# Optimization experiments

Hardware: AMD Instinct MI355X
Metric: run time of the kernel (lower is better)

Reference implementation:

```python
import jax, jax.numpy as jnp
import numpy as np

B, S, D, H = 1, 2048, 4096, 32
NEG = -1e9  # stands in for jnp.NINF in the source; finite to avoid NaNs in fully-masked rows


def _rope_tables(seq_len, dim):
    # cos/sin tables spanning the FULL hidden dim (RoPE here is applied pre-head-split)
    inv_freq = 1.0 / (10000.0 ** (np.arange(0, dim // 2, dtype=np.float32) / (dim // 2)))
    t = np.arange(seq_len, dtype=np.float32)
    freqs = np.outer(t, inv_freq)            # (S, D/2)
    emb = np.concatenate([freqs, freqs], -1)  # (S, D)
    return np.cos(emb)[None], np.sin(emb)[None]  # (1, S, D)


def setup_inputs() -> dict:
    key = jax.random.key(0)
    ks = jax.random.split(key, 5)
    cos, sin = _rope_tables(S, D)
    return {
        "hidden_state": jax.random.normal(ks[0], (B, S, D), jnp.float32),
        "attn_mask": jnp.zeros((B, 1, S, S), jnp.float32),
        "cos": jnp.asarray(cos),
        "sin": jnp.asarray(sin),
        "wq": jax.random.normal(ks[1], (D, D), jnp.float32) * 0.02,
        "wk": jax.random.normal(ks[2], (D, D), jnp.float32) * 0.02,
        "wv": jax.random.normal(ks[3], (D, D), jnp.float32) * 0.02,
        "wo": jax.random.normal(ks[4], (D, D), jnp.float32) * 0.02,
    }


def _rotate_half(x):
    x1, x2 = x[..., : x.shape[-1] // 2], x[..., x.shape[-1] // 2 :]
    return jnp.concatenate((-x2, x1), axis=-1)


def reference(hidden_state, attn_mask, cos, sin, wq, wk, wv, wo):
    b, s, d = hidden_state.shape
    h, hd = H, d // H
    # QKV projections (no bias), RoPE applied over the full hidden dim (pre-split, as in source)
    q = hidden_state @ wq
    k = hidden_state @ wk
    v = hidden_state @ wv
    q = q * cos + _rotate_half(q) * sin
    k = k * cos + _rotate_half(k) * sin
    split = lambda x: jnp.transpose(x.reshape(b, s, h, hd), (0, 2, 1, 3))  # (b,h,s,hd)
    q, k, v = split(q), split(k), split(v)
    # NOTE: source scales by sqrt(full hidden d), not sqrt(head_dim)
    scores = jnp.einsum("bhqd,bhkd->bhqk", q, k) / jnp.sqrt(jnp.float32(d))
    # source masks the LOWER triangle (incl. diagonal); replicated faithfully with finite NEG
    tri = jnp.tri(s, s, dtype=jnp.float32)
    mask = jnp.where(tri == 1, NEG, 0.0)[None, None]  # (1,1,s,s)
    scores = scores + attn_mask + mask
    attn = jax.nn.softmax(scores, axis=-1)
    out = jnp.einsum("bhqk,bhkd->bhqd", attn, v)
    out = jnp.transpose(out, (0, 2, 1, 3)).reshape(b, s, d)
    return out @ wo
```

## Files before the change

kernel.cpp:

```cpp
#include <hip/hip_runtime.h>
#include <stdint.h>


#define SS 2048
#define DD 4096
#define NH 32
#define HD 128
#define NEGV -1000000000.0f
#define LDP 136
#define LDV 72

typedef __bf16 bf16x8 __attribute__((ext_vector_type(8)));
typedef float f32x4 __attribute__((ext_vector_type(4)));

#define GLDS16(gp, lp)                                                        \
    __builtin_amdgcn_global_load_lds(                                         \
        (__attribute__((address_space(1))) uint32_t*)(uintptr_t)(gp),         \
        (__attribute__((address_space(3))) uint32_t*)(uintptr_t)(lp), 16, 0, 0)

__device__ __forceinline__ float bf2f(uint16_t u) {
    union { uint32_t i; float f; } v; v.i = ((uint32_t)u) << 16; return v.f;
}
__device__ __forceinline__ uint16_t f2bf(float f) {
    union { float f; uint32_t i; } v; v.f = f;
    uint32_t x = v.i;
    uint32_t r = (x + 0x7fffu + ((x >> 16) & 1u)) >> 16;
    return (uint16_t)r;
}

__device__ __forceinline__ void storeOut(float* C, size_t i, float v) { C[i] = v; }
__device__ __forceinline__ void storeOut(uint16_t* C, size_t i, float v) { C[i] = f2bf(v); }

__global__ void xconv_kernel(const float* __restrict__ in, uint16_t* __restrict__ out) {
    int i = blockIdx.x * blockDim.x + threadIdx.x;
    const float4* in4 = (const float4*)in;
    float4 a = in4[2 * i], b = in4[2 * i + 1];
    uint4 o;
    o.x = (uint32_t)f2bf(a.x) | ((uint32_t)f2bf(a.y) << 16);
    o.y = (uint32_t)f2bf(a.z) | ((uint32_t)f2bf(a.w) << 16);
    o.z = (uint32_t)f2bf(b.x) | ((uint32_t)f2bf(b.y) << 16);
    o.w = (uint32_t)f2bf(b.z) | ((uint32_t)f2bf(b.w) << 16);
    ((uint4*)out)[i] = o;
}

__global__ void wtrans_kernel(const float* __restrict__ in,
                              uint16_t* __restrict__ out) {
    __shared__ uint16_t tile[32][33];
    int bx = blockIdx.x * 32, by = blockIdx.y * 32;
    int tx = threadIdx.x, ty = threadIdx.y;
    #pragma unroll
    for (int i = 0; i < 32; i += 8)
        tile[ty + i][tx] = f2bf(in[(size_t)(by + ty + i) * DD + bx + tx]);
    __syncthreads();
    #pragma unroll
    for (int i = 0; i < 32; i += 8)
        out[(size_t)(bx + ty + i) * DD + by + tx] = tile[tx][ty + i];
}

template <typename OutT>
__global__ __launch_bounds__(256) void gemm_bt(const uint16_t* __restrict__ A,
                                               const uint16_t* __restrict__ Bt,
                                               OutT* __restrict__ C,
                                               int M, int N, int K) {
    __shared__ __attribute__((aligned(16))) uint16_t sA[128 * 32];
    __shared__ __attribute__((aligned(16))) uint16_t sB[128 * 32];
    int t = threadIdx.x;
    int lane = t & 63, w = t >> 6;
    int wm = (w >> 1) * 64, wn = (w & 1) * 64;
    int rowBase = blockIdx.y * 128, colBase = blockIdx.x * 128;
    f32x4 acc[4][4] = {};

    int lr = lane & 15;
    int kq = (lane >> 4) * 8;

    for (int k0 = 0; k0 < K; k0 += 32) {
        __syncthreads();
        #pragma unroll
        for (int p = 0; p < 2; ++p) {
            int c = p * 256 + t;
            int r = c >> 2;
            int cc = (c & 3) * 8;
            GLDS16(&A[(size_t)(rowBase + r) * K + k0 + cc], &sA[c * 8]);
            GLDS16(&Bt[(size_t)(colBase + r) * K + k0 + cc], &sB[c * 8]);
        }
        __syncthreads();

        bf16x8 af[4], bfr[4];
        #pragma unroll
        for (int i = 0; i < 4; ++i) {
            af[i]  = *(const bf16x8*)(&sA[(wm + i * 16 + lr) * 32 + kq]);
            bfr[i] = *(const bf16x8*)(&sB[(wn + i * 16 + lr) * 32 + kq]);
        }
        #pragma unroll
        for (int mt = 0; mt < 4; ++mt)
            #pragma unroll
            for (int nt = 0; nt < 4; ++nt)
                acc[mt][nt] = __builtin_amdgcn_mfma_f32_16x16x32_bf16(
                    af[mt], bfr[nt], acc[mt][nt], 0, 0, 0);
    }

    int q = lane >> 4;
    #pragma unroll
    for (int mt = 0; mt < 4; ++mt)
        #pragma unroll
        for (int nt = 0; nt < 4; ++nt)
            #pragma unroll
            for (int r = 0; r < 4; ++r) {
                int row = rowBase + wm + mt * 16 + q * 4 + r;
                int col = colBase + wn + nt * 16 + lr;
                storeOut(C, (size_t)row * N + col, acc[mt][nt][r]);
            }
}

__global__ void rope_kernel(uint16_t* __restrict__ q, uint16_t* __restrict__ k,
                            const float* __restrict__ cosb,
                            const float* __restrict__ sinb) {
    int idx = blockIdx.x * blockDim.x + threadIdx.x;
    int s = idx >> 11;
    int d = idx & 2047;
    size_t i0 = (size_t)s * DD + d, i1 = i0 + 2048;
    float c0 = cosb[i0], c1 = cosb[i1];
    float s0 = sinb[i0], s1 = sinb[i1];
    float q0 = bf2f(q[i0]), q1 = bf2f(q[i1]);
    q[i0] = f2bf(q0 * c0 - q1 * s0);
    q[i1] = f2bf(q1 * c1 + q0 * s1);
    float k0 = bf2f(k[i0]), k1 = bf2f(k[i1]);
    k[i0] = f2bf(k0 * c0 - k1 * s0);
    k[i1] = f2bf(k1 * c1 + k0 * s1);
}

__global__ __launch_bounds__(256) void fattn_kernel(
    const uint16_t* __restrict__ Q, const uint16_t* __restrict__ K,
    const uint16_t* __restrict__ VT, const float* __restrict__ mask,
    uint16_t* __restrict__ O)
{
    __shared__ __attribute__((aligned(16))) uint16_t sQ[64 * LDP];
    __shared__ __attribute__((aligned(16))) uint16_t sK[64 * LDP];
    __shared__ __attribute__((aligned(16))) uint16_t sVt[HD * LDV];
    __shared__ __attribute__((aligned(16))) uint16_t sP[64 * LDV];
    __shared__ float sAlpha[64];
    __shared__ float sL[64];

    int h = blockIdx.y, q0 = blockIdx.x * 64;
    int base = h * HD;
    int t = threadIdx.x;
    int lane = t & 63, w = t >> 6;
    int lr = lane & 15, quad = lane >> 4;
    int mw = w * 16;

    for (int c = t; c < 64 * 16; c += 256) {
        int m = c >> 4, dc = (c & 15) * 8;
        *(uint4*)(&sQ[m * LDP + dc]) =
            *(const uint4*)(&Q[(size_t)(q0 + m) * DD + base + dc]);
    }

    f32x4 oacc[2][4] = {};
    float m_pr[4], l_run[4];
    #pragma unroll
    for (int r = 0; r < 4; ++r) { m_pr[r] = -3.0e38f; l_run[r] = 0.f; }

    int kt_lo = (q0 == SS - 64) ? 0 : blockIdx.x;
    for (int kt = kt_lo; kt < SS / 64; ++kt) {
        __syncthreads();
        for (int c = t; c < 64 * 16; c += 256) {
            int r = c >> 4, dc = (c & 15) * 8;
            *(uint4*)(&sK[r * LDP + dc]) =
                *(const uint4*)(&K[(size_t)(kt * 64 + r) * DD + base + dc]);
        }
        for (int c = t; c < 128 * 8; c += 256) {
            int r = c >> 3, dc = (c & 7) * 8;
            *(uint4*)(&sVt[r * LDV + dc]) =
                *(const uint4*)(&VT[(size_t)(base + r) * SS + kt * 64 + dc]);
        }
        __syncthreads();

        f32x4 sacc[4] = {};
        __builtin_amdgcn_s_setprio(1);
        #pragma unroll
        for (int kc = 0; kc < 4; ++kc) {
            bf16x8 af = *(const bf16x8*)(&sQ[(mw + lr) * LDP + kc * 32 + quad * 8]);
            #pragma unroll
            for (int nt = 0; nt < 4; ++nt) {
                bf16x8 bfr = *(const bf16x8*)(&sK[(nt * 16 + lr) * LDP + kc * 32 + quad * 8]);
                sacc[nt] = __builtin_amdgcn_mfma_f32_16x16x32_bf16(af, bfr, sacc[nt], 0, 0, 0);
            }
        }
        __builtin_amdgcn_s_setprio(0);

        float sc[4][4];
        #pragma unroll
        for (int nt = 0; nt < 4; ++nt) {
            int kk = kt * 64 + nt * 16 + lr;
            #pragma unroll
            for (int r = 0; r < 4; ++r) {
                int qrow = q0 + mw + quad * 4 + r;
                float s = sacc[nt][r] * 0.015625f + mask[(size_t)qrow * SS + kk];
                if (kk <= qrow) s += NEGV;
                sc[nt][r] = s;
            }
        }

        float mnew[4], alpha[4];
        #pragma unroll
        for (int r = 0; r < 4; ++r) {
            float mx = sc[0][r];
            #pragma unroll
            for (int nt = 1; nt < 4; ++nt) mx = fmaxf(mx, sc[nt][r]);
            #pragma unroll
            for (int off = 1; off < 16; off <<= 1)
                mx = fmaxf(mx, __shfl_xor(mx, off));
            mnew[r] = fmaxf(m_pr[r], mx);
            alpha[r] = __expf(m_pr[r] - mnew[r]);
            m_pr[r] = mnew[r];
        }

        float ps[4] = {0.f, 0.f, 0.f, 0.f};
        #pragma unroll
        for (int nt = 0; nt < 4; ++nt) {
            #pragma unroll
            for (int r = 0; r < 4; ++r) {
                float p = __expf(sc[nt][r] - mnew[r]);
                ps[r] += p;
                sP[(mw + quad * 4 + r) * LDV + nt * 16 + lr] = f2bf(p);
            }
        }
        #pragma unroll
        for (int r = 0; r < 4; ++r) {
            #pragma unroll
            for (int off = 1; off < 16; off <<= 1)
                ps[r] += __shfl_xor(ps[r], off);
            l_run[r] = l_run[r] * alpha[r] + ps[r];
            if (lr == 0) sAlpha[mw + quad * 4 + r] = alpha[r];
        }
        __syncthreads();

        float a_col[4];
        #pragma unroll
        for (int nt = 0; nt < 4; ++nt) a_col[nt] = sAlpha[nt * 16 + lr];
        #pragma unroll
        for (int dt = 0; dt < 2; ++dt)
            #pragma unroll
            for (int nt = 0; nt < 4; ++nt)
                #pragma unroll
                for (int r = 0; r < 4; ++r)
                    oacc[dt][nt][r] *= a_col[nt];
        __builtin_amdgcn_s_setprio(1);
        #pragma unroll
        for (int kc = 0; kc < 2; ++kc) {
            bf16x8 bfr[4];
            #pragma unroll
            for (int nt = 0; nt < 4; ++nt)
                bfr[nt] = *(const bf16x8*)(&sP[(nt * 16 + lr) * LDV + kc * 32 + quad * 8]);
            #pragma unroll
            for (int dt = 0; dt < 2; ++dt) {
                bf16x8 af = *(const bf16x8*)(&sVt[((2 * w + dt) * 16 + lr) * LDV + kc * 32 + quad * 8]);
                #pragma unroll
                for (int nt = 0; nt < 4; ++nt)
                    oacc[dt][nt] = __builtin_amdgcn_mfma_f32_16x16x32_bf16(af, bfr[nt], oacc[dt][nt], 0, 0, 0);
            }
        }
        __builtin_amdgcn_s_setprio(0);
    }

    #pragma unroll
    for (int r = 0; r < 4; ++r)
        if (lr == 0) sL[mw + quad * 4 + r] = l_run[r];
    __syncthreads();

    float linv[4];
    #pragma unroll
    for (int nt = 0; nt < 4; ++nt) linv[nt] = 1.f / sL[nt * 16 + lr];
    #pragma unroll
    for (int dt = 0; dt < 2; ++dt) {
        int ddl = (2 * w + dt) * 16 + quad * 4;
        #pragma unroll
        for (int nt = 0; nt < 4; ++nt) {
            int ml = nt * 16 + lr;
            #pragma unroll
            for (int r = 0; r < 4; ++r)
                sK[ml * LDP + ddl + r] = f2bf(oacc[dt][nt][r] * linv[nt]);
        }
    }
    __syncthreads();
    for (int c = t; c < 64 * 16; c += 256) {
        int m = c >> 4, dc = (c & 15) * 8;
        *(uint4*)(&O[(size_t)(q0 + m) * DD + base + dc]) =
            *(const uint4*)(&sK[m * LDP + dc]);
    }
}

extern "C" void kernel_launch(void* const* d_in, const int* in_sizes, int n_in,
                              void* d_out, int out_size, void* d_ws, size_t ws_size,
                              hipStream_t stream) {
    const float* X    = (const float*)d_in[0];
    const float* mask = (const float*)d_in[1];
    const float* cosb = (const float*)d_in[2];
    const float* sinb = (const float*)d_in[3];
    const float* wq   = (const float*)d_in[4];
    const float* wk   = (const float*)d_in[5];
    const float* wv   = (const float*)d_in[6];
    const float* wo   = (const float*)d_in[7];
    float* out = (float*)d_out;

    char* ws = (char*)d_ws;
    uint16_t* Wt  = (uint16_t*)ws;
    uint16_t* Xbf = (uint16_t*)(ws + (size_t)33554432);
    uint16_t* Q   = Xbf + (size_t)SS * DD;
    uint16_t* Kb  = Q  + (size_t)SS * DD;
    uint16_t* VT  = Kb + (size_t)SS * DD;
    uint16_t* AO  = Xbf;

    dim3 tgrid(DD / 32, DD / 32), tblock(32, 8);
    dim3 ggrid(DD / 128, SS / 128), gblock(256);

    xconv_kernel<<<(SS * DD) / (256 * 8), 256, 0, stream>>>(X, Xbf);

    wtrans_kernel<<<tgrid, tblock, 0, stream>>>(wq, Wt);
    gemm_bt<<<ggrid, gblock, 0, stream>>>(Xbf, Wt, Q, SS, DD, DD);
    wtrans_kernel<<<tgrid, tblock, 0, stream>>>(wk, Wt);
    gemm_bt<<<ggrid, gblock, 0, stream>>>(Xbf, Wt, Kb, SS, DD, DD);
    wtrans_kernel<<<tgrid, tblock, 0, stream>>>(wv, Wt);
    gemm_bt<<<dim3(SS / 128, DD / 128), gblock, 0, stream>>>(Wt, Xbf, VT, DD, SS, DD);

    rope_kernel<<<(SS * 2048) / 256, 256, 0, stream>>>(Q, Kb, cosb, sinb);

    fattn_kernel<<<dim3(SS / 64, NH), 256, 0, stream>>>(Q, Kb, VT, mask, AO);

    wtrans_kernel<<<tgrid, tblock, 0, stream>>>(wo, Wt);
    gemm_bt<<<ggrid, gblock, 0, stream>>>(AO, Wt, out, SS, DD, DD);
}
```

Before: 1.111 ms.

## Pair causal query blocks per workgroup and stage mask tiles in LDS

Attention blocks now each handle two query tiles chosen as complementary pairs (j and 29-j, plus 30/31 together), so every workgroup does a similar amount of key-tile work under the triangular mask. The grid shrinks to 512 one-dimensional workgroups with a block-index swizzle spread across XCDs. The additive mask tile is also loaded into LDS with coalesced float4 loads instead of strided per-element global reads. This costs extra LDS (about 17 KB) and half as many workgroups in flight, which may lower occupancy.

```diff
diff --git a/kernel.cpp b/kernel.cpp
--- a/kernel.cpp
+++ b/kernel.cpp
@@ -9,6 +9,7 @@
 #define NEGV -1000000000.0f
 #define LDP 136
 #define LDV 72
+#define LDM 68
 
 typedef __bf16 bf16x8 __attribute__((ext_vector_type(8)));
 typedef float f32x4 __attribute__((ext_vector_type(4)));
@@ -138,154 +139,167 @@
     __shared__ __attribute__((aligned(16))) uint16_t sK[64 * LDP];
     __shared__ __attribute__((aligned(16))) uint16_t sVt[HD * LDV];
     __shared__ __attribute__((aligned(16))) uint16_t sP[64 * LDV];
+    __shared__ __attribute__((aligned(16))) float sM[64 * LDM];
     __shared__ float sAlpha[64];
     __shared__ float sL[64];
 
-    int h = blockIdx.y, q0 = blockIdx.x * 64;
+    int p = blockIdx.x;
+    int virt = (p & 7) * 64 + (p >> 3);
+    int h = virt >> 4, j = virt & 15;
     int base = h * HD;
     int t = threadIdx.x;
     int lane = t & 63, w = t >> 6;
     int lr = lane & 15, quad = lane >> 4;
     int mw = w * 16;
 
-    for (int c = t; c < 64 * 16; c += 256) {
-        int m = c >> 4, dc = (c & 15) * 8;
-        *(uint4*)(&sQ[m * LDP + dc]) =
-            *(const uint4*)(&Q[(size_t)(q0 + m) * DD + base + dc]);
-    }
-
-    f32x4 oacc[2][4] = {};
-    float m_pr[4], l_run[4];
-    #pragma unroll
-    for (int r = 0; r < 4; ++r) { m_pr[r] = -3.0e38f; l_run[r] = 0.f; }
-
-    int kt_lo = (q0 == SS - 64) ? 0 : blockIdx.x;
-    for (int kt = kt_lo; kt < SS / 64; ++kt) {
+    for (int item = 0; item < 2; ++item) {
+        int qb = (j < 15) ? (item ? 29 - j : j) : (30 + item);
+        int q0 = qb * 64;
+
+        for (int c = t; c < 64 * 16; c += 256) {
+            int m = c >> 4, dc = (c & 15) * 8;
+            *(uint4*)(&sQ[m * LDP + dc]) =
+                *(const uint4*)(&Q[(size_t)(q0 + m) * DD + base + dc]);
+        }
+
+        f32x4 oacc[2][4] = {};
+        float m_pr[4], l_run[4];
+        #pragma unroll
+        for (int r = 0; r < 4; ++r) { m_pr[r] = -3.0e38f; l_run[r] = 0.f; }
+
+        int kt_lo = (qb == 31) ? 0 : qb;
+        for (int kt = kt_lo; kt < SS / 64; ++kt) {
+            __syncthreads();
+            for (int c = t; c < 64 * 16; c += 256) {
+                int r = c >> 4, dc = (c & 15) * 8;
+                *(uint4*)(&sK[r * LDP + dc]) =
+                    *(const uint4*)(&K[(size_t)(kt * 64 + r) * DD + base + dc]);
+            }
+            for (int c = t; c < 128 * 8; c += 256) {
+                int r = c >> 3, dc = (c & 7) * 8;
+                *(uint4*)(&sVt[r * LDV + dc]) =
+                    *(const uint4*)(&VT[(size_t)(base + r) * SS + kt * 64 + dc]);
+            }
+            for (int c = t; c < 1024; c += 256) {
+                int r = c >> 4, c4 = (c & 15) * 4;
+                *(float4*)(&sM[r * LDM + c4]) =
+                    *(const float4*)(&mask[(size_t)(q0 + r) * SS + kt * 64 + c4]);
+            }
+            __syncthreads();
+
+            f32x4 sacc[4] = {};
+            __builtin_amdgcn_s_setprio(1);
+            #pragma unroll
+            for (int kc = 0; kc < 4; ++kc) {
+                bf16x8 af = *(const bf16x8*)(&sQ[(mw + lr) * LDP + kc * 32 + quad * 8]);
+                #pragma unroll
+                for (int nt = 0; nt < 4; ++nt) {
+                    bf16x8 bfr = *(const bf16x8*)(&sK[(nt * 16 + lr) * LDP + kc * 32 + quad * 8]);
+                    sacc[nt] = __builtin_amdgcn_mfma_f32_16x16x32_bf16(af, bfr, sacc[nt], 0, 0, 0);
+                }
+            }
+            __builtin_amdgcn_s_setprio(0);
+
+            float sc[4][4];
+            #pragma unroll
+            for (int nt = 0; nt < 4; ++nt) {
+                int kk = kt * 64 + nt * 16 + lr;
+                #pragma unroll
+                for (int r = 0; r < 4; ++r) {
+                    int qrl = mw + quad * 4 + r;
+                    float s = sacc[nt][r] * 0.015625f + sM[qrl * LDM + nt * 16 + lr];
+                    if (kk <= q0 + qrl) s += NEGV;
+                    sc[nt][r] = s;
+                }
+            }
+
+            float mnew[4], alpha[4];
+            #pragma unroll
+            for (int r = 0; r < 4; ++r) {
+                float mx = sc[0][r];
+                #pragma unroll
+                for (int nt = 1; nt < 4; ++nt) mx = fmaxf(mx, sc[nt][r]);
+                #pragma unroll
+                for (int off = 1; off < 16; off <<= 1)
+                    mx = fmaxf(mx, __shfl_xor(mx, off));
+                mnew[r] = fmaxf(m_pr[r], mx);
+                alpha[r] = __expf(m_pr[r] - mnew[r]);
+                m_pr[r] = mnew[r];
+            }
+
+            float ps[4] = {0.f, 0.f, 0.f, 0.f};
+            #pragma unroll
+            for (int nt = 0; nt < 4; ++nt) {
+                #pragma unroll
+                for (int r = 0; r < 4; ++r) {
+                    float pv = __expf(sc[nt][r] - mnew[r]);
+                    ps[r] += pv;
+                    sP[(mw + quad * 4 + r) * LDV + nt * 16 + lr] = f2bf(pv);
+                }
+            }
+            #pragma unroll
+            for (int r = 0; r < 4; ++r) {
+                #pragma unroll
+                for (int off = 1; off < 16; off <<= 1)
+                    ps[r] += __shfl_xor(ps[r], off);
+                l_run[r] = l_run[r] * alpha[r] + ps[r];
+                if (lr == 0) sAlpha[mw + quad * 4 + r] = alpha[r];
+            }
+            __syncthreads();
+
+            float a_col[4];
+            #pragma unroll
+            for (int nt = 0; nt < 4; ++nt) a_col[nt] = sAlpha[nt * 16 + lr];
+            #pragma unroll
+            for (int dt = 0; dt < 2; ++dt)
+                #pragma unroll
+                for (int nt = 0; nt < 4; ++nt)
+                    #pragma unroll
+                    for (int r = 0; r < 4; ++r)
+                        oacc[dt][nt][r] *= a_col[nt];
+            __builtin_amdgcn_s_setprio(1);
+            #pragma unroll
+            for (int kc = 0; kc < 2; ++kc) {
+                bf16x8 bfr[4];
+                #pragma unroll
+                for (int nt = 0; nt < 4; ++nt)
+                    bfr[nt] = *(const bf16x8*)(&sP[(nt * 16 + lr) * LDV + kc * 32 + quad * 8]);
+                #pragma unroll
+                for (int dt = 0; dt < 2; ++dt) {
+                    bf16x8 af = *(const bf16x8*)(&sVt[((2 * w + dt) * 16 + lr) * LDV + kc * 32 + quad * 8]);
+                    #pragma unroll
+                    for (int nt = 0; nt < 4; ++nt)
+                        oacc[dt][nt] = __builtin_amdgcn_mfma_f32_16x16x32_bf16(af, bfr[nt], oacc[dt][nt], 0, 0, 0);
+                }
+            }
+            __builtin_amdgcn_s_setprio(0);
+        }
+
+        #pragma unroll
+        for (int r = 0; r < 4; ++r)
+            if (lr == 0) sL[mw + quad * 4 + r] = l_run[r];
+        __syncthreads();
+
+        float linv[4];
+        #pragma unroll
+        for (int nt = 0; nt < 4; ++nt) linv[nt] = 1.f / sL[nt * 16 + lr];
+        #pragma unroll
+        for (int dt = 0; dt < 2; ++dt) {
+            int ddl = (2 * w + dt) * 16 + quad * 4;
+            #pragma unroll
+            for (int nt = 0; nt < 4; ++nt) {
+                int ml = nt * 16 + lr;
+                #pragma unroll
+                for (int r = 0; r < 4; ++r)
+                    sK[ml * LDP + ddl + r] = f2bf(oacc[dt][nt][r] * linv[nt]);
+            }
+        }
         __syncthreads();
         for (int c = t; c < 64 * 16; c += 256) {
-            int r = c >> 4, dc = (c & 15) * 8;
-            *(uint4*)(&sK[r * LDP + dc]) =
-                *(const uint4*)(&K[(size_t)(kt * 64 + r) * DD + base + dc]);
-        }
-        for (int c = t; c < 128 * 8; c += 256) {
-            int r = c >> 3, dc = (c & 7) * 8;
-            *(uint4*)(&sVt[r * LDV + dc]) =
-                *(const uint4*)(&VT[(size_t)(base + r) * SS + kt * 64 + dc]);
-        }
-        __syncthreads();
-
-        f32x4 sacc[4] = {};
-        __builtin_amdgcn_s_setprio(1);
-        #pragma unroll
-        for (int kc = 0; kc < 4; ++kc) {
-            bf16x8 af = *(const bf16x8*)(&sQ[(mw + lr) * LDP + kc * 32 + quad * 8]);
-            #pragma unroll
-            for (int nt = 0; nt < 4; ++nt) {
-                bf16x8 bfr = *(const bf16x8*)(&sK[(nt * 16 + lr) * LDP + kc * 32 + quad * 8]);
-                sacc[nt] = __builtin_amdgcn_mfma_f32_16x16x32_bf16(af, bfr, sacc[nt], 0, 0, 0);
-            }
-        }
-        __builtin_amdgcn_s_setprio(0);
-
-        float sc[4][4];
-        #pragma unroll
-        for (int nt = 0; nt < 4; ++nt) {
-            int kk = kt * 64 + nt * 16 + lr;
-            #pragma unroll
-            for (int r = 0; r < 4; ++r) {
-                int qrow = q0 + mw + quad * 4 + r;
-                float s = sacc[nt][r] * 0.015625f + mask[(size_t)qrow * SS + kk];
-                if (kk <= qrow) s += NEGV;
-                sc[nt][r] = s;
-            }
-        }
-
-        float mnew[4], alpha[4];
-        #pragma unroll
-        for (int r = 0; r < 4; ++r) {
-            float mx = sc[0][r];
-            #pragma unroll
-            for (int nt = 1; nt < 4; ++nt) mx = fmaxf(mx, sc[nt][r]);
-            #pragma unroll
-            for (int off = 1; off < 16; off <<= 1)
-                mx = fmaxf(mx, __shfl_xor(mx, off));
-            mnew[r] = fmaxf(m_pr[r], mx);
-            alpha[r] = __expf(m_pr[r] - mnew[r]);
-            m_pr[r] = mnew[r];
-        }
-
-        float ps[4] = {0.f, 0.f, 0.f, 0.f};
-        #pragma unroll
-        for (int nt = 0; nt < 4; ++nt) {
-            #pragma unroll
-            for (int r = 0; r < 4; ++r) {
-                float p = __expf(sc[nt][r] - mnew[r]);
-                ps[r] += p;
-                sP[(mw + quad * 4 + r) * LDV + nt * 16 + lr] = f2bf(p);
-            }
-        }
-        #pragma unroll
-        for (int r = 0; r < 4; ++r) {
-            #pragma unroll
-            for (int off = 1; off < 16; off <<= 1)
-                ps[r] += __shfl_xor(ps[r], off);
-            l_run[r] = l_run[r] * alpha[r] + ps[r];
-            if (lr == 0) sAlpha[mw + quad * 4 + r] = alpha[r];
-        }
-        __syncthreads();
-
-        float a_col[4];
-        #pragma unroll
-        for (int nt = 0; nt < 4; ++nt) a_col[nt] = sAlpha[nt * 16 + lr];
-        #pragma unroll
-        for (int dt = 0; dt < 2; ++dt)
-            #pragma unroll
-            for (int nt = 0; nt < 4; ++nt)
-                #pragma unroll
-                for (int r = 0; r < 4; ++r)
-                    oacc[dt][nt][r] *= a_col[nt];
-        __builtin_amdgcn_s_setprio(1);
-        #pragma unroll
-        for (int kc = 0; kc < 2; ++kc) {
-            bf16x8 bfr[4];
-            #pragma unroll
-            for (int nt = 0; nt < 4; ++nt)
-                bfr[nt] = *(const bf16x8*)(&sP[(nt * 16 + lr) * LDV + kc * 32 + quad * 8]);
-            #pragma unroll
-            for (int dt = 0; dt < 2; ++dt) {
-                bf16x8 af = *(const bf16x8*)(&sVt[((2 * w + dt) * 16 + lr) * LDV + kc * 32 + quad * 8]);
-                #pragma unroll
-                for (int nt = 0; nt < 4; ++nt)
-                    oacc[dt][nt] = __builtin_amdgcn_mfma_f32_16x16x32_bf16(af, bfr[nt], oacc[dt][nt], 0, 0, 0);
-            }
-        }
-        __builtin_amdgcn_s_setprio(0);
-    }
-
-    #pragma unroll
-    for (int r = 0; r < 4; ++r)
-        if (lr == 0) sL[mw + quad * 4 + r] = l_run[r];
-    __syncthreads();
-
-    float linv[4];
-    #pragma unroll
-    for (int nt = 0; nt < 4; ++nt) linv[nt] = 1.f / sL[nt * 16 + lr];
-    #pragma unroll
-    for (int dt = 0; dt < 2; ++dt) {
-        int ddl = (2 * w + dt) * 16 + quad * 4;
-        #pragma unroll
-        for (int nt = 0; nt < 4; ++nt) {
-            int ml = nt * 16 + lr;
-            #pragma unroll
-            for (int r = 0; r < 4; ++r)
-                sK[ml * LDP + ddl + r] = f2bf(oacc[dt][nt][r] * linv[nt]);
-        }
-    }
-    __syncthreads();
-    for (int c = t; c < 64 * 16; c += 256) {
-        int m = c >> 4, dc = (c & 15) * 8;
-        *(uint4*)(&O[(size_t)(q0 + m) * DD + base + dc]) =
-            *(const uint4*)(&sK[m * LDP + dc]);
+            int m = c >> 4, dc = (c & 15) * 8;
+            *(uint4*)(&O[(size_t)(q0 + m) * DD + base + dc]) =
+                *(const uint4*)(&sK[m * LDP + dc]);
+        }
     }
 }
 
@@ -324,7 +338,7 @@
 
     rope_kernel<<<(SS * 2048) / 256, 256, 0, stream>>>(Q, Kb, cosb, sinb);
 
-    fattn_kernel<<<dim3(SS / 64, NH), 256, 0, stream>>>(Q, Kb, VT, mask, AO);
+    fattn_kernel<<<dim3(512), 256, 0, stream>>>(Q, Kb, VT, mask, AO);
 
     wtrans_kernel<<<tgrid, tblock, 0, stream>>>(wo, Wt);
     gemm_bt<<<ggrid, gblock, 0, stream>>>(AO, Wt, out, SS, DD, DD);
```

Measured after the change: 983.1 us. -11.5%, faster.
